# Optimization experiments

Measured on AMD Instinct MI355X. Metric: run time of the kernel, lower is better.

## Reference

```python
import jax, jax.numpy as jnp
import numpy as np

B, N, C, H = 4, 1024, 1024, 16
DH = C // H  # 64
EPS = 1e-5   # nn.LayerNorm default


def _layernorm(x, g, b):
    m = x.mean(-1, keepdims=True)
    v = ((x - m) ** 2).mean(-1, keepdims=True)
    return (x - m) * jax.lax.rsqrt(v + EPS) * g + b


def _rot_half(x):
    d = x.shape[-1] // 2
    return jnp.concatenate([-x[..., d:], x[..., :d]], axis=-1)


def _apply_rope_cat(x, emb):
    # emb: [N, 2*DH] = sin || cos (torch tensor_split(2, -1) order)
    sin, cos = jnp.split(emb, 2, axis=-1)  # each [N, DH]
    return x * cos + _rot_half(x) * sin


def setup_inputs() -> dict:
    key = jax.random.key(0)
    ks = jax.random.split(key, 12)
    s = 0.02
    x = jax.random.normal(ks[0], (B, N, C), jnp.float32)
    delta_t_emb = jax.random.normal(ks[1], (B, N, C), jnp.float32)
    v_residual_v1 = jax.random.normal(ks[2], (B, H, N, DH), jnp.float32)
    # realistic rope table: sin||cos, each DH wide (freqs repeated twice for rotate_half)
    pos = jnp.arange(N, dtype=jnp.float32)
    inv_freq = 1.0 / (10000.0 ** (jnp.arange(0, DH // 2, dtype=jnp.float32) / (DH // 2)))
    freqs = pos[:, None] * inv_freq[None, :]          # [N, DH/2]
    freqs = jnp.concatenate([freqs, freqs], axis=-1)  # [N, DH]
    rope = jnp.concatenate([jnp.sin(freqs), jnp.cos(freqs)], axis=-1)  # [N, 2*DH]
    Wqkv = jax.random.normal(ks[3], (3 * C, C), jnp.float32) * s
    bqkv = jnp.zeros((3 * C,), jnp.float32)
    Wdt = jax.random.normal(ks[4], (3 * C, C), jnp.float32) * s
    bdt = jnp.zeros((3 * C,), jnp.float32)
    qn_g = jnp.ones((DH,), jnp.float32); qn_b = jnp.zeros((DH,), jnp.float32)
    kn_g = jnp.ones((DH,), jnp.float32); kn_b = jnp.zeros((DH,), jnp.float32)
    lamb1 = jnp.asarray(0.5, jnp.float32)
    lamb2 = jnp.asarray(0.5, jnp.float32)
    Wproj = jax.random.normal(ks[5], (C, C), jnp.float32) * s
    bproj = jnp.zeros((C,), jnp.float32)
    return {
        "x": x, "rope": rope, "delta_t_emb": delta_t_emb, "v_residual_v1": v_residual_v1,
        "Wqkv": Wqkv, "bqkv": bqkv, "Wdt": Wdt, "bdt": bdt,
        "qn_g": qn_g, "qn_b": qn_b, "kn_g": kn_g, "kn_b": kn_b,
        "lamb1": lamb1, "lamb2": lamb2, "Wproj": Wproj, "bproj": bproj,
    }


def reference(x, rope, delta_t_emb, v_residual_v1, Wqkv, bqkv, Wdt, bdt,
              qn_g, qn_b, kn_g, kn_b, lamb1, lamb2, Wproj, bproj):
    b, n, c = x.shape
    # fused QKV: [B,N,3C] -> [3,B,H,N,DH]
    qkv = (jnp.einsum('bnc,oc->bno', x, Wqkv) + bqkv).reshape(b, n, 3, H, DH)
    qkv = jnp.transpose(qkv, (2, 0, 3, 1, 4))
    q, k, v = qkv[0], qkv[1], qkv[2]
    # delta-t additive embeddings
    dqkv = (jnp.einsum('bnc,oc->bno', delta_t_emb, Wdt) + bdt).reshape(b, n, 3, H, DH)
    dqkv = jnp.transpose(dqkv, (2, 0, 3, 1, 4))
    q = q + dqkv[0]; k = k + dqkv[1]; v = v + dqkv[2]
    # value-residual mixing
    v = lamb1 * v + lamb2 * v_residual_v1
    # qk layernorm over head_dim
    q = _layernorm(q, qn_g, qn_b)
    k = _layernorm(k, kn_g, kn_b)
    # RoPE (num_prefix_tokens = 0, rotate_half=True)
    q = _apply_rope_cat(q, rope)
    k = _apply_rope_cat(k, rope)
    # SDPA, non-causal, no dropout
    scale = 1.0 / jnp.sqrt(jnp.asarray(DH, x.dtype))
    scores = jnp.einsum('bhqd,bhkd->bhqk', q, k) * scale
    attn = jax.nn.softmax(scores, axis=-1)
    out = jnp.einsum('bhqk,bhkd->bhqd', attn, v)
    # [B,H,N,DH] -> [B,N,C], output norm is Identity (scale_norm=False)
    out = jnp.transpose(out, (0, 2, 1, 3)).reshape(b, n, c)
    out = jnp.einsum('bnc,oc->bno', out, Wproj) + bproj
    return out
```

## Files before the change

kernel.cpp:

```cpp
#include <hip/hip_runtime.h>
#include <stdint.h>

typedef unsigned short u16;
typedef __attribute__((ext_vector_type(8))) short short8;
typedef __attribute__((ext_vector_type(4))) float f32x4;
typedef __attribute__((ext_vector_type(4))) unsigned short u16x4;
typedef __attribute__((ext_vector_type(4))) unsigned int u32x4;

#define DEVI __device__ __forceinline__

DEVI u16 f2bf(float f) {
  uint32_t u = __builtin_bit_cast(uint32_t, f);
  u += 0x7fffu + ((u >> 16) & 1u);
  return (u16)(u >> 16);
}

DEVI float bf2f(u16 u) {
  uint32_t v = ((uint32_t)u) << 16;
  return __builtin_bit_cast(float, v);
}

DEVI uint32_t cvt_pk_bf16(float lo, float hi) {
  uint32_t r;
  asm("v_cvt_pk_bf16_f32 %0, %1, %2" : "=v"(r) : "v"(lo), "v"(hi));
  return r;
}

DEVI void gload_lds16(const void* g, void* l) {
  __builtin_amdgcn_global_load_lds(
      (const __attribute__((address_space(1))) void*)g,
      (__attribute__((address_space(3))) void*)(uint32_t)(uintptr_t)l,
      16, 0, 0);
}

__global__ void cvt_all(const float* __restrict__ x, const float* __restrict__ dte,
                        const float* __restrict__ Wqkv, const float* __restrict__ Wdt,
                        const float* __restrict__ Wproj,
                        u16* __restrict__ A_cat, u16* __restrict__ W_cat,
                        u16* __restrict__ Wp) {
  const long T0 = (long)4096 * 2048 / 4;
  const long T1 = (long)3072 * 2048 / 4;
  const long T2 = (long)1024 * 1024 / 4;
  for (long v = (long)blockIdx.x * 256 + threadIdx.x; v < T0 + T1 + T2;
       v += (long)gridDim.x * 256) {
    const float* src;
    u16* dst;
    if (v < T0) {
      const long i = v * 4;
      const long row = i >> 11, c = i & 2047;
      src = (c < 1024) ? (x + row * 1024 + c) : (dte + row * 1024 + (c - 1024));
      dst = A_cat + i;
    } else if (v < T0 + T1) {
      const long i = (v - T0) * 4;
      const long row = i >> 11, c = i & 2047;
      src = (c < 1024) ? (Wqkv + row * 1024 + c) : (Wdt + row * 1024 + (c - 1024));
      dst = W_cat + i;
    } else {
      const long i = (v - T0 - T1) * 4;
      src = Wproj + i;
      dst = Wp + i;
    }
    const float4 f = *(const float4*)src;
    u16x4 o = {f2bf(f.x), f2bf(f.y), f2bf(f.z), f2bf(f.w)};
    *(u16x4*)dst = o;
  }
}

__global__ __launch_bounds__(256, 2)
void gemm_bt64(const u16* __restrict__ A, const u16* __restrict__ B,
               float* __restrict__ C, const float* __restrict__ bias1,
               int M, int N, int K) {
  __shared__ u16 As[64 * 32];
  __shared__ u16 Bs[128 * 32];
  const int t = threadIdx.x;
  const int w = t >> 6, l = t & 63;
  const int l15 = l & 15, lg = l >> 4;
  const int bm = blockIdx.x, bn = blockIdx.y;
  const int wr = (w >> 1) * 32, wc = (w & 1) * 64;
  f32x4 acc[2][4] = {};
  const int su = (l & 7) ^ (l >> 3);
  const int rsub = 2 * (l >> 3) + (su >> 2);
  const int sg = su & 3;
  const int sfr = (lg + 4 * (l15 & 1)) ^ (l15 >> 1);
  const int lh = l15 >> 1;

  for (int kt = 0; kt < (K >> 5); ++kt) {
    {
      const int r = w * 16 + rsub;
      gload_lds16(A + (long)(bm * 64 + r) * K + kt * 32 + sg * 8,
                  (char*)As + (w * 8) * 128);
    }
#pragma unroll
    for (int i = 0; i < 2; ++i) {
      const int r = i * 64 + w * 16 + rsub;
      gload_lds16(B + (long)(bn * 128 + r) * K + kt * 32 + sg * 8,
                  (char*)Bs + (i * 32 + w * 8) * 128);
    }
    __syncthreads();
    short8 af[2], bfr[4];
#pragma unroll
    for (int m = 0; m < 2; ++m)
      af[m] = *(const short8*)&As[((w >> 1) * 16 + m * 8 + lh) * 64 + sfr * 8];
#pragma unroll
    for (int n = 0; n < 4; ++n)
      bfr[n] = *(const short8*)&Bs[((w & 1) * 32 + n * 8 + lh) * 64 + sfr * 8];
#pragma unroll
    for (int m = 0; m < 2; ++m)
#pragma unroll
      for (int n = 0; n < 4; ++n)
        acc[m][n] = __builtin_amdgcn_mfma_f32_16x16x32_bf16(af[m], bfr[n], acc[m][n], 0, 0, 0);
    __syncthreads();
  }
#pragma unroll
  for (int m = 0; m < 2; ++m) {
    const int row0 = bm * 64 + wr + m * 16 + lg * 4;
#pragma unroll
    for (int n = 0; n < 4; ++n) {
      const int col = bn * 128 + wc + n * 16 + l15;
      const float bia = bias1 ? bias1[col] : 0.f;
#pragma unroll
      for (int r = 0; r < 4; ++r)
        C[(long)(row0 + r) * N + col] = acc[m][n][r] + bia;
    }
  }
}

__global__ __launch_bounds__(256, 2)
void gemm_qkv_hm(const u16* __restrict__ A, const u16* __restrict__ B,
                 const float* __restrict__ bias1, const float* __restrict__ bias2,
                 u16* __restrict__ Qraw, u16* __restrict__ Kraw,
                 u16* __restrict__ Vraw, int M, int N, int K) {
  __shared__ u16 As[128 * 32];
  __shared__ u16 Bs[128 * 32];
  const int t = threadIdx.x;
  const int w = t >> 6, l = t & 63;
  const int l15 = l & 15, lg = l >> 4;
  const int bm = blockIdx.x, bn = blockIdx.y;
  const int wc = (w & 1) * 64;
  const int wrh = (w >> 1) * 32, wch = (w & 1) * 32;
  f32x4 acc[4][4] = {};
  const int su = (l & 7) ^ (l >> 3);
  const int rsub = 2 * (l >> 3) + (su >> 2);
  const int sg = su & 3;
  const int sfr = (lg + 4 * (l15 & 1)) ^ (l15 >> 1);
  const int lh = l15 >> 1;

  for (int kt = 0; kt < (K >> 5); ++kt) {
#pragma unroll
    for (int i = 0; i < 2; ++i) {
      const int r = i * 64 + w * 16 + rsub;
      gload_lds16(A + (long)(bm * 128 + r) * K + kt * 32 + sg * 8,
                  (char*)As + (i * 32 + w * 8) * 128);
      gload_lds16(B + (long)(bn * 128 + r) * K + kt * 32 + sg * 8,
                  (char*)Bs + (i * 32 + w * 8) * 128);
    }
    __syncthreads();
    short8 af[4], bfr[4];
#pragma unroll
    for (int m = 0; m < 4; ++m)
      af[m] = *(const short8*)&As[(wrh + m * 8 + lh) * 64 + sfr * 8];
#pragma unroll
    for (int n = 0; n < 4; ++n)
      bfr[n] = *(const short8*)&Bs[(wch + n * 8 + lh) * 64 + sfr * 8];
#pragma unroll
    for (int m = 0; m < 4; ++m)
#pragma unroll
      for (int n = 0; n < 4; ++n)
        acc[m][n] = __builtin_amdgcn_mfma_f32_16x16x32_bf16(af[m], bfr[n], acc[m][n], 0, 0, 0);
    __syncthreads();
  }
  u16* Traw = (bn < 8) ? Qraw : (bn < 16) ? Kraw : Vraw;
  const int h = ((bn & 7) << 1) | (wc >> 6);
  const long tb = ((long)((bm >> 3) * 16 + h)) << 16;
  const int nnbase = (bm & 7) * 128 + (w >> 1) * 64;
#pragma unroll
  for (int m = 0; m < 4; ++m) {
#pragma unroll
    for (int n = 0; n < 4; ++n) {
      const int col = bn * 128 + wc + n * 16 + l15;
      float bia = bias1[col] + bias2[col];
      const int d = n * 16 + l15;
#pragma unroll
      for (int r = 0; r < 4; ++r) {
        const int nn = nnbase + m * 16 + lg * 4 + r;
        Traw[tb + (long)nn * 64 + d] = f2bf(acc[m][n][r] + bia);
      }
    }
  }
}

__global__ __launch_bounds__(256)
void fuse_kv(const u16* __restrict__ Kraw, const u16* __restrict__ Vraw,
             const float* __restrict__ vres, const float* __restrict__ rope,
             const float* __restrict__ kg, const float* __restrict__ kb,
             const float* __restrict__ pl1, const float* __restrict__ pl2,
             u16* __restrict__ Ksw, u16* __restrict__ VTsw) {
  __shared__ u16 Vl[64][72];
  const int t = threadIdx.x, w = t >> 6, l = t & 63;
  const int c4 = l & 3;
  const int tg = l >> 2;
  const int d0 = c4 * 8;
  const int bh = blockIdx.x, ntile = blockIdx.y;
  const int n0 = ntile * 64;
  const int tl = w * 16 + tg;
  const int n = n0 + tl;
  const long obase = (long)bh * 65536 + (long)n * 64;
  const int nx = n & 7;

  {
    const short8 xlo = *(const short8*)&Kraw[obase + d0];
    const short8 xhi = *(const short8*)&Kraw[obase + 32 + d0];
    float vlo[8], vhi[8];
    float s = 0.f;
#pragma unroll
    for (int u = 0; u < 8; ++u) {
      vlo[u] = bf2f((u16)xlo[u]);
      vhi[u] = bf2f((u16)xhi[u]);
      s += vlo[u] + vhi[u];
    }
    s += __shfl_xor(s, 1); s += __shfl_xor(s, 2);
    const float mean = s * (1.f / 64.f);
    float vs = 0.f;
#pragma unroll
    for (int u = 0; u < 8; ++u) {
      vlo[u] -= mean; vhi[u] -= mean;
      vs += vlo[u] * vlo[u] + vhi[u] * vhi[u];
    }
    vs += __shfl_xor(vs, 1); vs += __shfl_xor(vs, 2);
    const float rstd = 1.f / sqrtf(vs * (1.f / 64.f) + 1e-5f);
    u32x4 plo, phi;
#pragma unroll
    for (int p2 = 0; p2 < 2; ++p2) {
      const int db = p2 * 4;
      const float4 gl = *(const float4*)&kg[d0 + db];
      const float4 bl = *(const float4*)&kb[d0 + db];
      const float4 gh = *(const float4*)&kg[32 + d0 + db];
      const float4 bhh = *(const float4*)&kb[32 + d0 + db];
      const float4 snl = *(const float4*)&rope[n * 128 + d0 + db];
      const float4 snh = *(const float4*)&rope[n * 128 + 32 + d0 + db];
      const float4 csl = *(const float4*)&rope[n * 128 + 64 + d0 + db];
      const float4 csh = *(const float4*)&rope[n * 128 + 96 + d0 + db];
      float ol[4], oh[4];
#pragma unroll
      for (int u = 0; u < 4; ++u) {
        const float nl_ = vlo[db + u] * rstd * ((const float*)&gl)[u] + ((const float*)&bl)[u];
        const float nh_ = vhi[db + u] * rstd * ((const float*)&gh)[u] + ((const float*)&bhh)[u];
        ol[u] = nl_ * ((const float*)&csl)[u] - nh_ * ((const float*)&snl)[u];
        oh[u] = nh_ * ((const float*)&csh)[u] + nl_ * ((const float*)&snh)[u];
      }
      plo[p2 * 2] = cvt_pk_bf16(ol[0], ol[1]);
      plo[p2 * 2 + 1] = cvt_pk_bf16(ol[2], ol[3]);
      phi[p2 * 2] = cvt_pk_bf16(oh[0], oh[1]);
      phi[p2 * 2 + 1] = cvt_pk_bf16(oh[2], oh[3]);
    }
    *(u32x4*)&Ksw[obase + ((c4 ^ nx) * 8)] = plo;
    *(u32x4*)&Ksw[obase + (((c4 + 4) ^ nx) * 8)] = phi;
  }

  {
    const float l1 = pl1[0], l2 = pl2[0];
    const short8 xlo = *(const short8*)&Vraw[obase + d0];
    const short8 xhi = *(const short8*)&Vraw[obase + 32 + d0];
    const long vb = ((long)(bh * 1024 + n)) * 64;
    const float4 r0 = *(const float4*)&vres[vb + d0];
    const float4 r1 = *(const float4*)&vres[vb + d0 + 4];
    const float4 r2 = *(const float4*)&vres[vb + 32 + d0];
    const float4 r3 = *(const float4*)&vres[vb + 32 + d0 + 4];
    const float rl[8] = {r0.x, r0.y, r0.z, r0.w, r1.x, r1.y, r1.z, r1.w};
    const float rh[8] = {r2.x, r2.y, r2.z, r2.w, r3.x, r3.y, r3.z, r3.w};
    u32x4 plo, phi;
#pragma unroll
    for (int u = 0; u < 4; ++u) {
      plo[u] = cvt_pk_bf16(l1 * bf2f((u16)xlo[2 * u]) + l2 * rl[2 * u],
                           l1 * bf2f((u16)xlo[2 * u + 1]) + l2 * rl[2 * u + 1]);
      phi[u] = cvt_pk_bf16(l1 * bf2f((u16)xhi[2 * u]) + l2 * rh[2 * u],
                           l1 * bf2f((u16)xhi[2 * u + 1]) + l2 * rh[2 * u + 1]);
    }
    *(u32x4*)&Vl[tl][d0] = plo;
    *(u32x4*)&Vl[tl][32 + d0] = phi;
  }
  __syncthreads();
#pragma unroll
  for (int i = 0; i < 2; ++i) {
    const int task = i * 256 + t;
    const int dd = task >> 3, cc = task & 7;
    short8 o;
#pragma unroll
    for (int u = 0; u < 8; ++u) o[u] = (short)Vl[cc * 8 + u][dd];
    *(short8*)&VTsw[((long)(bh * 64 + dd)) * 1024 + n0 + ((cc ^ (dd & 7)) * 8)] = o;
  }
}

__global__ __launch_bounds__(256, 4)
void attn_fwd9(const u16* __restrict__ Qraw, const u16* __restrict__ Ksw,
               const u16* __restrict__ VTsw, const float* __restrict__ rope,
               const float* __restrict__ qg, const float* __restrict__ qb,
               u16* __restrict__ Out) {
  __shared__ u16 Kl[128 * 64];
  __shared__ u16 Vl[64 * 128];
  const int t = threadIdx.x, w = t >> 6, l = t & 63;
  const int l15 = l & 15, lg = l >> 4;
  const int x7 = l15 & 7;
  const int bh = blockIdx.x, q0 = blockIdx.y * 64;
  const long bo = (long)bh * 65536;
  const bool hihalf = (l & 16) != 0;

  const int qrow = q0 + w * 16 + l15;
  short8 qf[2];
  {
    const int dq = lg * 8;
    const long qb_ = bo + (long)qrow * 64;
    const short8 x0 = *(const short8*)&Qraw[qb_ + dq];
    const short8 x1 = *(const short8*)&Qraw[qb_ + 32 + dq];
    float v0[8], v1[8];
    float s = 0.f;
#pragma unroll
    for (int u = 0; u < 8; ++u) {
      v0[u] = bf2f((u16)x0[u]);
      v1[u] = bf2f((u16)x1[u]);
      s += v0[u] + v1[u];
    }
    s += __shfl_xor(s, 16); s += __shfl_xor(s, 32);
    const float mean = s * (1.f / 64.f);
    float vs = 0.f;
#pragma unroll
    for (int u = 0; u < 8; ++u) {
      v0[u] -= mean; v1[u] -= mean;
      vs += v0[u] * v0[u] + v1[u] * v1[u];
    }
    vs += __shfl_xor(vs, 16); vs += __shfl_xor(vs, 32);
    const float rstd = 1.f / sqrtf(vs * (1.f / 64.f) + 1e-5f);
    u32x4 p0, p1;
#pragma unroll
    for (int p2 = 0; p2 < 2; ++p2) {
      const int db = p2 * 4;
      const float4 gl = *(const float4*)&qg[dq + db];
      const float4 bl = *(const float4*)&qb[dq + db];
      const float4 gh = *(const float4*)&qg[32 + dq + db];
      const float4 bhh = *(const float4*)&qb[32 + dq + db];
      const float4 snl = *(const float4*)&rope[qrow * 128 + dq + db];
      const float4 snh = *(const float4*)&rope[qrow * 128 + 32 + dq + db];
      const float4 csl = *(const float4*)&rope[qrow * 128 + 64 + dq + db];
      const float4 csh = *(const float4*)&rope[qrow * 128 + 96 + dq + db];
      float ol[4], oh[4];
#pragma unroll
      for (int u = 0; u < 4; ++u) {
        const float nl_ = v0[db + u] * rstd * ((const float*)&gl)[u] + ((const float*)&bl)[u];
        const float nh_ = v1[db + u] * rstd * ((const float*)&gh)[u] + ((const float*)&bhh)[u];
        ol[u] = nl_ * ((const float*)&csl)[u] - nh_ * ((const float*)&snl)[u];
        oh[u] = nh_ * ((const float*)&csh)[u] + nl_ * ((const float*)&snh)[u];
      }
      p0[p2 * 2] = cvt_pk_bf16(ol[0], ol[1]);
      p0[p2 * 2 + 1] = cvt_pk_bf16(ol[2], ol[3]);
      p1[p2 * 2] = cvt_pk_bf16(oh[0], oh[1]);
      p1[p2 * 2 + 1] = cvt_pk_bf16(oh[2], oh[3]);
    }
    qf[0] = __builtin_bit_cast(short8, p0);
    qf[1] = __builtin_bit_cast(short8, p1);
  }

  f32x4 acc[4] = {};
  float m_run = -1e30f, l_run = 0.f;

  for (int kb = 0; kb < 8; ++kb) {
    const int kvb = kb * 128;
#pragma unroll
    for (int i = 0; i < 4; ++i) {
      const int idx = i * 256 + t;
      const int krow = idx >> 3, kseg = idx & 7;
      gload_lds16(Ksw + bo + (long)(kvb + krow) * 64 + kseg * 8, (char*)Kl + idx * 16);
      const int vd = idx >> 4, vc = idx & 15;
      gload_lds16(VTsw + bo + (long)vd * 1024 + kvb + vc * 8,
                  (char*)Vl + vd * 256 + vc * 16);
    }
    __syncthreads();
#pragma unroll
    for (int tb = 0; tb < 2; ++tb) {
      f32x4 p[4];
#pragma unroll
      for (int mt = 0; mt < 4; ++mt) {
        f32x4 ps = {};
#pragma unroll
        for (int ks = 0; ks < 2; ++ks) {
          const short8 kf = *(const short8*)&Kl[(tb * 64 + mt * 16 + l15) * 64 +
                                                (((ks * 4 + lg) ^ x7) * 8)];
          ps = __builtin_amdgcn_mfma_f32_16x16x32_bf16(kf, qf[ks], ps, 0, 0, 0);
        }
        p[mt] = ps;
      }
      float mx = p[0][0];
#pragma unroll
      for (int mt = 0; mt < 4; ++mt)
#pragma unroll
        for (int r = 0; r < 4; ++r) mx = fmaxf(mx, p[mt][r]);
      mx = fmaxf(mx, __shfl_xor(mx, 16));
      mx = fmaxf(mx, __shfl_xor(mx, 32));
      const float mnew = fmaxf(m_run, mx * 0.125f);
      const float alpha = __expf(m_run - mnew);
      m_run = mnew;
      float sum = 0.f;
#pragma unroll
      for (int mt = 0; mt < 4; ++mt)
#pragma unroll
        for (int r = 0; r < 4; ++r) {
          const float e = __expf(p[mt][r] * 0.125f - mnew);
          p[mt][r] = e;
          sum += e;
        }
      sum += __shfl_xor(sum, 16);
      sum += __shfl_xor(sum, 32);
      l_run = l_run * alpha + sum;
      uint32_t u0[4], u1[4];
#pragma unroll
      for (int mt = 0; mt < 4; ++mt) {
        u0[mt] = cvt_pk_bf16(p[mt][0], p[mt][1]);
        u1[mt] = cvt_pk_bf16(p[mt][2], p[mt][3]);
      }
#pragma unroll
      for (int mt = 0; mt < 4; ++mt)
#pragma unroll
        for (int r = 0; r < 4; ++r) acc[mt][r] *= alpha;
#pragma unroll
      for (int ks = 0; ks < 2; ++ks) {
        uint32_t X0 = u0[2 * ks], Y0 = u0[2 * ks + 1];
        asm("v_permlane32_swap_b32 %0, %1" : "+v"(X0), "+v"(Y0));
        uint32_t X1 = u1[2 * ks], Y1 = u1[2 * ks + 1];
        asm("v_permlane32_swap_b32 %0, %1" : "+v"(X1), "+v"(Y1));
        const uint32_t Xs0 = (uint32_t)__shfl_xor((int)X0, 16);
        const uint32_t Ys0 = (uint32_t)__shfl_xor((int)Y0, 16);
        const uint32_t Xs1 = (uint32_t)__shfl_xor((int)X1, 16);
        const uint32_t Ys1 = (uint32_t)__shfl_xor((int)Y1, 16);
        u32x4 pv;
        pv[0] = hihalf ? Ys0 : X0;
        pv[1] = hihalf ? Ys1 : X1;
        pv[2] = hihalf ? Y0 : Xs0;
        pv[3] = hihalf ? Y1 : Xs1;
        const short8 pf = __builtin_bit_cast(short8, pv);
#pragma unroll
        for (int mt = 0; mt < 4; ++mt) {
          const short8 vf = *(const short8*)&Vl[(mt * 16 + l15) * 128 + tb * 64 +
                                                (((ks * 4 + lg) ^ x7) * 8)];
          acc[mt] = __builtin_amdgcn_mfma_f32_16x16x32_bf16(vf, pf, acc[mt], 0, 0, 0);
        }
      }
    }
    __syncthreads();
  }
  const int b = bh >> 4, h = bh & 15;
  const float inv = 1.f / l_run;
  const long obase = ((long)(b * 1024 + qrow)) * 1024 + h * 64;
#pragma unroll
  for (int mt = 0; mt < 4; ++mt) {
    const long o = obase + mt * 16 + lg * 4;
    *(uint32_t*)&Out[o] = cvt_pk_bf16(acc[mt][0] * inv, acc[mt][1] * inv);
    *(uint32_t*)&Out[o + 2] = cvt_pk_bf16(acc[mt][2] * inv, acc[mt][3] * inv);
  }
}

extern "C" void kernel_launch(void* const* d_in, const int* in_sizes, int n_in,
                              void* d_out, int out_size, void* d_ws, size_t ws_size,
                              hipStream_t stream) {
  const float* x     = (const float*)d_in[0];
  const float* rope  = (const float*)d_in[1];
  const float* dte   = (const float*)d_in[2];
  const float* vres  = (const float*)d_in[3];
  const float* Wqkv  = (const float*)d_in[4];
  const float* bqkv  = (const float*)d_in[5];
  const float* Wdt   = (const float*)d_in[6];
  const float* bdt   = (const float*)d_in[7];
  const float* qn_g  = (const float*)d_in[8];
  const float* qn_b  = (const float*)d_in[9];
  const float* kn_g  = (const float*)d_in[10];
  const float* kn_b  = (const float*)d_in[11];
  const float* l1    = (const float*)d_in[12];
  const float* l2    = (const float*)d_in[13];
  const float* Wproj = (const float*)d_in[14];
  const float* bproj = (const float*)d_in[15];
  float* out = (float*)d_out;

  char* ws = (char*)d_ws;
  u16*   A_cat = (u16*)(ws);
  u16*   W_cat = (u16*)(ws + 16777216);
  u16*   Wp    = (u16*)(ws + 29360128);
  u16*   Qraw  = (u16*)(ws + 31457280);
  u16*   Kraw  = (u16*)(ws + 39845888);
  u16*   Vraw  = (u16*)(ws + 48234496);
  u16*   Ksw   = (u16*)(ws + 65011712);
  u16*   VTsw  = (u16*)(ws + 73400320);
  u16*   AO    = (u16*)(ws + 81788928);

  cvt_all<<<2048, 256, 0, stream>>>(x, dte, Wqkv, Wdt, Wproj, A_cat, W_cat, Wp);
  gemm_qkv_hm<<<dim3(32, 24), 256, 0, stream>>>(A_cat, W_cat, bqkv, bdt,
                                                Qraw, Kraw, Vraw, 4096, 3072, 2048);
  fuse_kv<<<dim3(64, 16), 256, 0, stream>>>(Kraw, Vraw, vres, rope, kn_g, kn_b,
                                            l1, l2, Ksw, VTsw);
  attn_fwd9<<<dim3(64, 16), 256, 0, stream>>>(Qraw, Ksw, VTsw, rope, qn_g, qn_b, AO);
  gemm_bt64<<<dim3(64, 8), 256, 0, stream>>>(AO, Wp, out, bproj, 4096, 1024, 1024);
}
```

Measured before the change: 147.4 us.

## Move K/V swizzle from fuse_kv writes to attention loads; loop tiles per block

The K/V preprocessing kernel now writes K and transposed V in plain row-major order, and the attention kernel applies the XOR swizzle on the global-load address side when filling LDS. The preprocessing kernel also processes four 64-row tiles per block, with gamma/beta hoisted into registers, so its grid shrinks fourfold. This is meant to make the preprocessing stores contiguous and cut per-block overhead. The cost is scattered 16-byte global reads in attention and fewer blocks in fuse_kv.

```diff
diff --git a/kernel.cpp b/kernel.cpp
--- a/kernel.cpp
+++ b/kernel.cpp
@@ -190,112 +190,118 @@
 }
 
 __global__ __launch_bounds__(256)
-void fuse_kv(const u16* __restrict__ Kraw, const u16* __restrict__ Vraw,
-             const float* __restrict__ vres, const float* __restrict__ rope,
-             const float* __restrict__ kg, const float* __restrict__ kb,
-             const float* __restrict__ pl1, const float* __restrict__ pl2,
-             u16* __restrict__ Ksw, u16* __restrict__ VTsw) {
+void fuse_kv2(const u16* __restrict__ Kraw, const u16* __restrict__ Vraw,
+              const float* __restrict__ vres, const float* __restrict__ rope,
+              const float* __restrict__ kg, const float* __restrict__ kb,
+              const float* __restrict__ pl1, const float* __restrict__ pl2,
+              u16* __restrict__ Ksw, u16* __restrict__ VT) {
   __shared__ u16 Vl[64][72];
   const int t = threadIdx.x, w = t >> 6, l = t & 63;
   const int c4 = l & 3;
   const int tg = l >> 2;
   const int d0 = c4 * 8;
-  const int bh = blockIdx.x, ntile = blockIdx.y;
-  const int n0 = ntile * 64;
-  const int tl = w * 16 + tg;
-  const int n = n0 + tl;
-  const long obase = (long)bh * 65536 + (long)n * 64;
-  const int nx = n & 7;
-
-  {
-    const short8 xlo = *(const short8*)&Kraw[obase + d0];
-    const short8 xhi = *(const short8*)&Kraw[obase + 32 + d0];
-    float vlo[8], vhi[8];
-    float s = 0.f;
-#pragma unroll
-    for (int u = 0; u < 8; ++u) {
-      vlo[u] = bf2f((u16)xlo[u]);
-      vhi[u] = bf2f((u16)xhi[u]);
-      s += vlo[u] + vhi[u];
-    }
-    s += __shfl_xor(s, 1); s += __shfl_xor(s, 2);
-    const float mean = s * (1.f / 64.f);
-    float vs = 0.f;
-#pragma unroll
-    for (int u = 0; u < 8; ++u) {
-      vlo[u] -= mean; vhi[u] -= mean;
-      vs += vlo[u] * vlo[u] + vhi[u] * vhi[u];
-    }
-    vs += __shfl_xor(vs, 1); vs += __shfl_xor(vs, 2);
-    const float rstd = 1.f / sqrtf(vs * (1.f / 64.f) + 1e-5f);
-    u32x4 plo, phi;
-#pragma unroll
-    for (int p2 = 0; p2 < 2; ++p2) {
-      const int db = p2 * 4;
-      const float4 gl = *(const float4*)&kg[d0 + db];
-      const float4 bl = *(const float4*)&kb[d0 + db];
-      const float4 gh = *(const float4*)&kg[32 + d0 + db];
-      const float4 bhh = *(const float4*)&kb[32 + d0 + db];
-      const float4 snl = *(const float4*)&rope[n * 128 + d0 + db];
-      const float4 snh = *(const float4*)&rope[n * 128 + 32 + d0 + db];
-      const float4 csl = *(const float4*)&rope[n * 128 + 64 + d0 + db];
-      const float4 csh = *(const float4*)&rope[n * 128 + 96 + d0 + db];
-      float ol[4], oh[4];
+  const int bh = blockIdx.x;
+  const float l1 = pl1[0], l2 = pl2[0];
+  float glo[8], blo[8], ghi[8], bhi[8];
+#pragma unroll
+  for (int u = 0; u < 8; ++u) {
+    glo[u] = kg[d0 + u];  blo[u] = kb[d0 + u];
+    ghi[u] = kg[32 + d0 + u]; bhi[u] = kb[32 + d0 + u];
+  }
+
+  for (int it = 0; it < 4; ++it) {
+    const int n0 = (blockIdx.y * 4 + it) * 64;
+    const int tl = w * 16 + tg;
+    const int n = n0 + tl;
+    const long obase = (long)bh * 65536 + (long)n * 64;
+
+    if (it) __syncthreads();
+
+    {
+      const short8 xlo = *(const short8*)&Kraw[obase + d0];
+      const short8 xhi = *(const short8*)&Kraw[obase + 32 + d0];
+      float vlo[8], vhi[8];
+      float s = 0.f;
+#pragma unroll
+      for (int u = 0; u < 8; ++u) {
+        vlo[u] = bf2f((u16)xlo[u]);
+        vhi[u] = bf2f((u16)xhi[u]);
+        s += vlo[u] + vhi[u];
+      }
+      s += __shfl_xor(s, 1); s += __shfl_xor(s, 2);
+      const float mean = s * (1.f / 64.f);
+      float vs = 0.f;
+#pragma unroll
+      for (int u = 0; u < 8; ++u) {
+        vlo[u] -= mean; vhi[u] -= mean;
+        vs += vlo[u] * vlo[u] + vhi[u] * vhi[u];
+      }
+      vs += __shfl_xor(vs, 1); vs += __shfl_xor(vs, 2);
+      const float rstd = 1.f / sqrtf(vs * (1.f / 64.f) + 1e-5f);
+      u32x4 plo, phi;
+#pragma unroll
+      for (int p2 = 0; p2 < 2; ++p2) {
+        const int db = p2 * 4;
+        const float4 snl = *(const float4*)&rope[n * 128 + d0 + db];
+        const float4 snh = *(const float4*)&rope[n * 128 + 32 + d0 + db];
+        const float4 csl = *(const float4*)&rope[n * 128 + 64 + d0 + db];
+        const float4 csh = *(const float4*)&rope[n * 128 + 96 + d0 + db];
+        float ol[4], oh[4];
+#pragma unroll
+        for (int u = 0; u < 4; ++u) {
+          const float nl_ = vlo[db + u] * rstd * glo[db + u] + blo[db + u];
+          const float nh_ = vhi[db + u] * rstd * ghi[db + u] + bhi[db + u];
+          ol[u] = nl_ * ((const float*)&csl)[u] - nh_ * ((const float*)&snl)[u];
+          oh[u] = nh_ * ((const float*)&csh)[u] + nl_ * ((const float*)&snh)[u];
+        }
+        plo[p2 * 2] = cvt_pk_bf16(ol[0], ol[1]);
+        plo[p2 * 2 + 1] = cvt_pk_bf16(ol[2], ol[3]);
+        phi[p2 * 2] = cvt_pk_bf16(oh[0], oh[1]);
+        phi[p2 * 2 + 1] = cvt_pk_bf16(oh[2], oh[3]);
+      }
+      *(u32x4*)&Ksw[obase + d0] = plo;
+      *(u32x4*)&Ksw[obase + 32 + d0] = phi;
+    }
+
+    {
+      const short8 xlo = *(const short8*)&Vraw[obase + d0];
+      const short8 xhi = *(const short8*)&Vraw[obase + 32 + d0];
+      const long vb = ((long)(bh * 1024 + n)) * 64;
+      const float4 r0 = *(const float4*)&vres[vb + d0];
+      const float4 r1 = *(const float4*)&vres[vb + d0 + 4];
+      const float4 r2 = *(const float4*)&vres[vb + 32 + d0];
+      const float4 r3 = *(const float4*)&vres[vb + 32 + d0 + 4];
+      const float rl[8] = {r0.x, r0.y, r0.z, r0.w, r1.x, r1.y, r1.z, r1.w};
+      const float rh[8] = {r2.x, r2.y, r2.z, r2.w, r3.x, r3.y, r3.z, r3.w};
+      u32x4 plo, phi;
 #pragma unroll
       for (int u = 0; u < 4; ++u) {
-        const float nl_ = vlo[db + u] * rstd * ((const float*)&gl)[u] + ((const float*)&bl)[u];
-        const float nh_ = vhi[db + u] * rstd * ((const float*)&gh)[u] + ((const float*)&bhh)[u];
-        ol[u] = nl_ * ((const float*)&csl)[u] - nh_ * ((const float*)&snl)[u];
-        oh[u] = nh_ * ((const float*)&csh)[u] + nl_ * ((const float*)&snh)[u];
-      }
-      plo[p2 * 2] = cvt_pk_bf16(ol[0], ol[1]);
-      plo[p2 * 2 + 1] = cvt_pk_bf16(ol[2], ol[3]);
-      phi[p2 * 2] = cvt_pk_bf16(oh[0], oh[1]);
-      phi[p2 * 2 + 1] = cvt_pk_bf16(oh[2], oh[3]);
-    }
-    *(u32x4*)&Ksw[obase + ((c4 ^ nx) * 8)] = plo;
-    *(u32x4*)&Ksw[obase + (((c4 + 4) ^ nx) * 8)] = phi;
-  }
-
-  {
-    const float l1 = pl1[0], l2 = pl2[0];
-    const short8 xlo = *(const short8*)&Vraw[obase + d0];
-    const short8 xhi = *(const short8*)&Vraw[obase + 32 + d0];
-    const long vb = ((long)(bh * 1024 + n)) * 64;
-    const float4 r0 = *(const float4*)&vres[vb + d0];
-    const float4 r1 = *(const float4*)&vres[vb + d0 + 4];
-    const float4 r2 = *(const float4*)&vres[vb + 32 + d0];
-    const float4 r3 = *(const float4*)&vres[vb + 32 + d0 + 4];
-    const float rl[8] = {r0.x, r0.y, r0.z, r0.w, r1.x, r1.y, r1.z, r1.w};
-    const float rh[8] = {r2.x, r2.y, r2.z, r2.w, r3.x, r3.y, r3.z, r3.w};
-    u32x4 plo, phi;
-#pragma unroll
-    for (int u = 0; u < 4; ++u) {
-      plo[u] = cvt_pk_bf16(l1 * bf2f((u16)xlo[2 * u]) + l2 * rl[2 * u],
-                           l1 * bf2f((u16)xlo[2 * u + 1]) + l2 * rl[2 * u + 1]);
-      phi[u] = cvt_pk_bf16(l1 * bf2f((u16)xhi[2 * u]) + l2 * rh[2 * u],
-                           l1 * bf2f((u16)xhi[2 * u + 1]) + l2 * rh[2 * u + 1]);
-    }
-    *(u32x4*)&Vl[tl][d0] = plo;
-    *(u32x4*)&Vl[tl][32 + d0] = phi;
-  }
-  __syncthreads();
-#pragma unroll
-  for (int i = 0; i < 2; ++i) {
-    const int task = i * 256 + t;
-    const int dd = task >> 3, cc = task & 7;
-    short8 o;
-#pragma unroll
-    for (int u = 0; u < 8; ++u) o[u] = (short)Vl[cc * 8 + u][dd];
-    *(short8*)&VTsw[((long)(bh * 64 + dd)) * 1024 + n0 + ((cc ^ (dd & 7)) * 8)] = o;
+        plo[u] = cvt_pk_bf16(l1 * bf2f((u16)xlo[2 * u]) + l2 * rl[2 * u],
+                             l1 * bf2f((u16)xlo[2 * u + 1]) + l2 * rl[2 * u + 1]);
+        phi[u] = cvt_pk_bf16(l1 * bf2f((u16)xhi[2 * u]) + l2 * rh[2 * u],
+                             l1 * bf2f((u16)xhi[2 * u + 1]) + l2 * rh[2 * u + 1]);
+      }
+      *(u32x4*)&Vl[tl][d0] = plo;
+      *(u32x4*)&Vl[tl][32 + d0] = phi;
+    }
+    __syncthreads();
+#pragma unroll
+    for (int i = 0; i < 2; ++i) {
+      const int task = i * 256 + t;
+      const int dd = task >> 3, cc = task & 7;
+      short8 o;
+#pragma unroll
+      for (int u = 0; u < 8; ++u) o[u] = (short)Vl[cc * 8 + u][dd];
+      *(short8*)&VT[((long)(bh * 64 + dd)) * 1024 + n0 + cc * 8] = o;
+    }
   }
 }
 
 __global__ __launch_bounds__(256, 4)
-void attn_fwd9(const u16* __restrict__ Qraw, const u16* __restrict__ Ksw,
-               const u16* __restrict__ VTsw, const float* __restrict__ rope,
-               const float* __restrict__ qg, const float* __restrict__ qb,
-               u16* __restrict__ Out) {
+void attn_fwd10(const u16* __restrict__ Qraw, const u16* __restrict__ Ksw,
+                const u16* __restrict__ VT, const float* __restrict__ rope,
+                const float* __restrict__ qg, const float* __restrict__ qb,
+                u16* __restrict__ Out) {
   __shared__ u16 Kl[128 * 64];
   __shared__ u16 Vl[64 * 128];
   const int t = threadIdx.x, w = t >> 6, l = t & 63;
@@ -368,9 +374,11 @@
     for (int i = 0; i < 4; ++i) {
       const int idx = i * 256 + t;
       const int krow = idx >> 3, kseg = idx & 7;
-      gload_lds16(Ksw + bo + (long)(kvb + krow) * 64 + kseg * 8, (char*)Kl + idx * 16);
+      gload_lds16(Ksw + bo + (long)(kvb + krow) * 64 + ((kseg ^ (krow & 7)) * 8),
+                  (char*)Kl + idx * 16);
       const int vd = idx >> 4, vc = idx & 15;
-      gload_lds16(VTsw + bo + (long)vd * 1024 + kvb + vc * 8,
+      gload_lds16(VT + bo + (long)vd * 1024 + kvb + (vc >> 3) * 64 +
+                      (((vc & 7) ^ (vd & 7)) * 8),
                   (char*)Vl + vd * 256 + vc * 16);
     }
     __syncthreads();
@@ -486,14 +494,14 @@
   u16*   Kraw  = (u16*)(ws + 39845888);
   u16*   Vraw  = (u16*)(ws + 48234496);
   u16*   Ksw   = (u16*)(ws + 65011712);
-  u16*   VTsw  = (u16*)(ws + 73400320);
+  u16*   VT    = (u16*)(ws + 73400320);
   u16*   AO    = (u16*)(ws + 81788928);
 
   cvt_all<<<2048, 256, 0, stream>>>(x, dte, Wqkv, Wdt, Wproj, A_cat, W_cat, Wp);
   gemm_qkv_hm<<<dim3(32, 24), 256, 0, stream>>>(A_cat, W_cat, bqkv, bdt,
                                                 Qraw, Kraw, Vraw, 4096, 3072, 2048);
-  fuse_kv<<<dim3(64, 16), 256, 0, stream>>>(Kraw, Vraw, vres, rope, kn_g, kn_b,
-                                            l1, l2, Ksw, VTsw);
-  attn_fwd9<<<dim3(64, 16), 256, 0, stream>>>(Qraw, Ksw, VTsw, rope, qn_g, qn_b, AO);
+  fuse_kv2<<<dim3(64, 4), 256, 0, stream>>>(Kraw, Vraw, vres, rope, kn_g, kn_b,
+                                            l1, l2, Ksw, VT);
+  attn_fwd10<<<dim3(64, 16), 256, 0, stream>>>(Qraw, Ksw, VT, rope, qn_g, qn_b, AO);
   gemm_bt64<<<dim3(64, 8), 256, 0, stream>>>(AO, Wp, out, bproj, 4096, 1024, 1024);
 }
```

New measurement: 149.0 us. About the same (+1.1%).
